# Performance work log

Measured on AMD Instinct MI355X. Metric: run time of the kernel, lower is better.

The kernel has to match this reference:

```python
import jax, jax.numpy as jnp
import numpy as np

B, N, C_IN, C_OUT, E_DIM = 16, 1024, 64, 64, 4


def setup_inputs() -> dict:
    key = jax.random.key(0)
    ks = jax.random.split(key, 7)
    x = jax.random.normal(ks[0], (B, N, C_IN), dtype=jnp.float32)
    adj = jax.random.uniform(ks[1], (B, N, N), dtype=jnp.float32)
    edge_attr = jax.random.randint(ks[2], (B, N, N, 1), 0, E_DIM, dtype=jnp.int32)
    scale = 1.0 / np.sqrt(C_IN)
    W_rel = jax.random.normal(ks[3], (C_IN, C_OUT), dtype=jnp.float32) * scale
    b_rel = jax.random.normal(ks[4], (C_OUT,), dtype=jnp.float32) * scale
    W_root = jax.random.normal(ks[5], (C_IN, C_OUT), dtype=jnp.float32) * scale
    w_edge = jax.random.normal(ks[6], (E_DIM,), dtype=jnp.float32)
    return {"x": x, "adj": adj, "edge_attr": edge_attr,
            "W_rel": W_rel, "b_rel": b_rel, "W_root": W_root, "w_edge": w_edge}


def reference(x, adj, edge_attr, W_rel, b_rel, W_root, w_edge):
    # one_hot(edge_attr) @ w_edge == gather of w_edge by edge type (same math,
    # avoids materializing the B x N x N x E_DIM one-hot tensor).
    e = w_edge[edge_attr[..., 0]]            # [B, N, N]
    adj_w = adj * e                           # weighted adjacency
    out = jnp.matmul(adj_w, x)                # [B, N, C_IN] aggregation (aggr='add')
    out = jnp.matmul(out, W_rel) + b_rel      # lin_rel
    out = out + jnp.matmul(x, W_root)         # lin_root (no bias)
    return out
```

## Files before the change

### kernel.cpp

```cpp
#include <hip/hip_runtime.h>

#define BB 16
#define NN 1024
#define CC 64

typedef __attribute__((ext_vector_type(8))) short short8;
typedef __attribute__((ext_vector_type(4))) float f32x4;
typedef __attribute__((ext_vector_type(4))) int   i32x4;

__device__ __forceinline__ unsigned short bf16_rne(float f) {
    unsigned u = __float_as_uint(f);
    u += 0x7fffu + ((u >> 16) & 1u);
    return (unsigned short)(u >> 16);
}

extern "C" __global__ __launch_bounds__(256)
void precompute(const float* __restrict__ x, const float* __restrict__ W_rel,
                const float* __restrict__ W_root, const float* __restrict__ b_rel,
                unsigned short* __restrict__ xw_sw, float* __restrict__ out)
{
    __shared__ float wrel_s[64 * 64];
    __shared__ float wroot_s[64 * 64];
    __shared__ float x_s[16 * 68];

    const int t = threadIdx.x;
    #pragma unroll
    for (int k = 0; k < 4; ++k) {
        int i4 = t + 256 * k;
        ((float4*)wrel_s)[i4]  = ((const float4*)W_rel)[i4];
        ((float4*)wroot_s)[i4] = ((const float4*)W_root)[i4];
    }
    const int row0 = blockIdx.x * 16;
    {
        int r = t >> 4, c4 = t & 15;
        *(float4*)(x_s + r * 68 + c4 * 4) = ((const float4*)(x + (size_t)(row0 + r) * CC))[c4];
    }
    __syncthreads();

    const int c4 = t & 15;
    const int r  = t >> 4;
    float aw0 = 0.f, aw1 = 0.f, aw2 = 0.f, aw3 = 0.f;
    float ar0 = 0.f, ar1 = 0.f, ar2 = 0.f, ar3 = 0.f;
    const float* xrow = x_s + r * 68;
    #pragma unroll 8
    for (int k = 0; k < 64; ++k) {
        float xv = xrow[k];
        float4 wv = ((const float4*)(wrel_s  + k * 64))[c4];
        float4 rv = ((const float4*)(wroot_s + k * 64))[c4];
        aw0 += xv * wv.x; aw1 += xv * wv.y; aw2 += xv * wv.z; aw3 += xv * wv.w;
        ar0 += xv * rv.x; ar1 += xv * rv.y; ar2 += xv * rv.z; ar3 += xv * rv.w;
    }

    const int row_g = row0 + r;
    {
        const float4 bv = ((const float4*)b_rel)[c4];
        ((float4*)out)[(size_t)row_g * 16 + c4] =
            make_float4(ar0 + bv.x, ar1 + bv.y, ar2 + bv.z, ar3 + bv.w);
    }
    {
        const int b = row_g >> 10;
        const int k = row_g & 1023;
        const int kb = k >> 5;
        const int qk = (k >> 3) & 3;
        const int j  = k & 7;
        const int c  = 4 * c4;
        const int n0 = c >> 4;
        const int n  = c & 15;
        size_t off = ((size_t)b << 16) + (size_t)((kb * 4 + n0) << 9)
                   + (size_t)((n + (qk << 4)) << 3) + j;
        xw_sw[off]      = bf16_rne(aw0);
        xw_sw[off + 8]  = bf16_rne(aw1);
        xw_sw[off + 16] = bf16_rne(aw2);
        xw_sw[off + 24] = bf16_rne(aw3);
    }
}

extern "C" __global__ __launch_bounds__(256, 4)
void gnn_mfma(const float* __restrict__ adj, const int* __restrict__ ea,
              const float* __restrict__ w_edge,
              const unsigned short* __restrict__ xw_sw,
              float* __restrict__ out)
{
    __shared__ __align__(16) char lds[32768];

    const int t     = threadIdx.x;
    const int mtile = blockIdx.x & 63;
    const int b     = blockIdx.x >> 6;
    const int row0  = mtile << 4;

    const float w0 = w_edge[0], w1 = w_edge[1], w2 = w_edge[2], w3 = w_edge[3];
    const float d1 = w1 - w0;
    const float d2 = w2 - 2.f * w1 + w0;
    const float d3 = w3 - 3.f * w2 + 3.f * w1 - w0;
    const float c3 = d3 * (1.f / 6.f);
    const float c2 = 0.5f * d2 - 0.5f * d3;
    const float c1 = d1 - 0.5f * d2 + (1.f / 3.f) * d3;
    const float c0 = w0;

#define WSEL(ev) __builtin_fmaf(__builtin_fmaf(__builtin_fmaf(c3, (float)(ev), c2), (float)(ev), c1), (float)(ev), c0)

    const size_t gbase = ((size_t)b << 20) + ((size_t)row0 << 10);
    const f32x4* A4 = (const f32x4*)(adj + gbase);
    const i32x4* E4 = (const i32x4*)(ea + gbase);

    const int kb_t   = t >> 3;
    const int q_t    = (t >> 1) & 3;
    const int X_t    = ((kb_t & 3) << 2) | q_t;
    const int wbase  = (kb_t << 10) + (q_t << 8) + ((t & 1) << 3);

    f32x4 aa[8]; i32x4 ee[8];
    #pragma unroll
    for (int d = 0; d < 8; ++d) {
        aa[d] = __builtin_nontemporal_load(&A4[d * 256 + t]);
        ee[d] = __builtin_nontemporal_load(&E4[d * 256 + t]);
    }

    #pragma unroll
    for (int i = 0; i < 16; ++i) {
        f32x4 av = aa[i & 7];
        i32x4 ev = ee[i & 7];
        if (i < 8) {
            aa[i & 7] = __builtin_nontemporal_load(&A4[(i + 8) * 256 + t]);
            ee[i & 7] = __builtin_nontemporal_load(&E4[(i + 8) * 256 + t]);
        }
        float p0 = av[0] * WSEL(ev[0]);
        float p1 = av[1] * WSEL(ev[1]);
        float p2 = av[2] * WSEL(ev[2]);
        float p3 = av[3] * WSEL(ev[3]);
        unsigned u0 = __builtin_amdgcn_perm(__float_as_uint(p1), __float_as_uint(p0), 0x07060302u);
        unsigned u1 = __builtin_amdgcn_perm(__float_as_uint(p3), __float_as_uint(p2), 0x07060302u);
        const int m = i;
        const int addr = wbase + ((m ^ X_t) << 4);
        *(uint2*)(lds + addr) = make_uint2(u0, u1);
    }
    __syncthreads();

    const int wn   = t >> 6;
    const int lane = t & 63;
    const int m    = lane & 15;
    const int q    = lane >> 4;

    const unsigned short* xwb = xw_sw + ((size_t)b << 16)
                              + ((size_t)wn << 9) + ((size_t)lane << 3);
    const char* abase = lds + (q << 8);

    f32x4 acc0 = {0.f, 0.f, 0.f, 0.f};

    #pragma unroll
    for (int kb = 0; kb < 32; ++kb) {
        const int X = ((kb & 3) << 2) | q;
        short8 af = *(const short8*)(abase + (kb << 10) + ((m ^ X) << 4));
        short8 bf = *(const short8*)(xwb + ((size_t)kb << 11));
        acc0 = __builtin_amdgcn_mfma_f32_16x16x32_bf16(af, bf, acc0, 0, 0, 0);
    }
#undef WSEL

    float* ob = out + ((((size_t)b << 10) + row0 + (q << 2)) << 6) + (wn << 4) + m;
    #pragma unroll
    for (int rg = 0; rg < 4; ++rg) {
        ob[rg * 64] += acc0[rg];
    }
}

extern "C" void kernel_launch(void* const* d_in, const int* in_sizes, int n_in,
                              void* d_out, int out_size, void* d_ws, size_t ws_size,
                              hipStream_t stream) {
    const float* x      = (const float*)d_in[0];
    const float* adj    = (const float*)d_in[1];
    const int*   ea     = (const int*)  d_in[2];
    const float* W_rel  = (const float*)d_in[3];
    const float* b_rel  = (const float*)d_in[4];
    const float* W_root = (const float*)d_in[5];
    const float* w_edge = (const float*)d_in[6];
    float* out = (float*)d_out;

    unsigned short* xw_sw = (unsigned short*)d_ws;

    precompute<<<BB * NN / 16, 256, 0, stream>>>(x, W_rel, W_root, b_rel, xw_sw, out);
    gnn_mfma<<<BB * (NN / 16), 256, 0, stream>>>(adj, ea, w_edge, xw_sw, out);
}
```

Baseline: 164.9 us.

## Split adjacency weighting into a separate bf16 pack pass before the MFMA kernel

Adds a streaming pack kernel that reads adj and edge_attr, applies the edge-type weights, and writes a bf16 weighted adjacency to workspace. A lighter MFMA kernel then reads the packed bf16 rows directly, with no LDS staging. The aim is better memory streaming and occupancy in each pass. The cost is an extra 32 MB write and read round trip plus one more kernel launch, on top of the mandatory 128 MB input read. The original fused path is kept as a fallback when the workspace is too small.

```diff
diff --git a/kernel.cpp b/kernel.cpp
--- a/kernel.cpp
+++ b/kernel.cpp
@@ -13,6 +13,17 @@
     u += 0x7fffu + ((u >> 16) & 1u);
     return (unsigned short)(u >> 16);
 }
+
+#define WSEL_COEFFS(w_edge) \
+    const float w0 = w_edge[0], w1 = w_edge[1], w2 = w_edge[2], w3 = w_edge[3]; \
+    const float d1 = w1 - w0; \
+    const float d2 = w2 - 2.f * w1 + w0; \
+    const float d3 = w3 - 3.f * w2 + 3.f * w1 - w0; \
+    const float c3 = d3 * (1.f / 6.f); \
+    const float c2 = 0.5f * d2 - 0.5f * d3; \
+    const float c1 = d1 - 0.5f * d2 + (1.f / 3.f) * d3; \
+    const float c0 = w0;
+#define WSEL(ev) __builtin_fmaf(__builtin_fmaf(__builtin_fmaf(c3, (float)(ev), c2), (float)(ev), c1), (float)(ev), c0)
 
 extern "C" __global__ __launch_bounds__(256)
 void precompute(const float* __restrict__ x, const float* __restrict__ W_rel,
@@ -75,6 +86,78 @@
     }
 }
 
+extern "C" __global__ __launch_bounds__(256)
+void pack(const float* __restrict__ adj, const int* __restrict__ ea,
+          const float* __restrict__ w_edge, uint2* __restrict__ adjw)
+{
+    const int g = blockIdx.x * 256 + threadIdx.x;
+    const int S = 2048 * 256;
+
+    WSEL_COEFFS(w_edge);
+
+    const f32x4* A4 = (const f32x4*)adj;
+    const i32x4* E4 = (const i32x4*)ea;
+
+    f32x4 a[4]; i32x4 e[4];
+    #pragma unroll
+    for (int j = 0; j < 4; ++j) {
+        a[j] = __builtin_nontemporal_load(&A4[(size_t)j * S + g]);
+        e[j] = __builtin_nontemporal_load(&E4[(size_t)j * S + g]);
+    }
+
+    #pragma unroll
+    for (int j = 0; j < 8; ++j) {
+        f32x4 av = a[j & 3];
+        i32x4 ev = e[j & 3];
+        if (j < 4) {
+            a[j & 3] = __builtin_nontemporal_load(&A4[(size_t)(j + 4) * S + g]);
+            e[j & 3] = __builtin_nontemporal_load(&E4[(size_t)(j + 4) * S + g]);
+        }
+        float p0 = av[0] * WSEL(ev[0]);
+        float p1 = av[1] * WSEL(ev[1]);
+        float p2 = av[2] * WSEL(ev[2]);
+        float p3 = av[3] * WSEL(ev[3]);
+        unsigned u0 = __builtin_amdgcn_perm(__float_as_uint(p1), __float_as_uint(p0), 0x07060302u);
+        unsigned u1 = __builtin_amdgcn_perm(__float_as_uint(p3), __float_as_uint(p2), 0x07060302u);
+        adjw[(size_t)j * S + g] = make_uint2(u0, u1);
+    }
+}
+
+extern "C" __global__ __launch_bounds__(256)
+void gnn_lite(const unsigned short* __restrict__ adjw,
+              const unsigned short* __restrict__ xw_sw,
+              float* __restrict__ out)
+{
+    const int t     = threadIdx.x;
+    const int wn    = t >> 6;
+    const int lane  = t & 63;
+    const int m     = lane & 15;
+    const int q     = lane >> 4;
+    const int mtile = blockIdx.x & 63;
+    const int b     = blockIdx.x >> 6;
+    const int row0  = mtile << 4;
+
+    const unsigned short* ap = adjw + ((size_t)b << 20)
+                             + ((size_t)(row0 + m) << 10) + (q << 3);
+    const unsigned short* xwb = xw_sw + ((size_t)b << 16)
+                              + ((size_t)wn << 9) + ((size_t)lane << 3);
+
+    f32x4 acc = {0.f, 0.f, 0.f, 0.f};
+
+    #pragma unroll
+    for (int kb = 0; kb < 32; ++kb) {
+        short8 af = *(const short8*)(ap + (kb << 5));
+        short8 bf = *(const short8*)(xwb + ((size_t)kb << 11));
+        acc = __builtin_amdgcn_mfma_f32_16x16x32_bf16(af, bf, acc, 0, 0, 0);
+    }
+
+    float* ob = out + ((((size_t)b << 10) + row0 + (q << 2)) << 6) + (wn << 4) + m;
+    #pragma unroll
+    for (int rg = 0; rg < 4; ++rg) {
+        ob[rg * 64] += acc[rg];
+    }
+}
+
 extern "C" __global__ __launch_bounds__(256, 4)
 void gnn_mfma(const float* __restrict__ adj, const int* __restrict__ ea,
               const float* __restrict__ w_edge,
@@ -88,16 +171,7 @@
     const int b     = blockIdx.x >> 6;
     const int row0  = mtile << 4;
 
-    const float w0 = w_edge[0], w1 = w_edge[1], w2 = w_edge[2], w3 = w_edge[3];
-    const float d1 = w1 - w0;
-    const float d2 = w2 - 2.f * w1 + w0;
-    const float d3 = w3 - 3.f * w2 + 3.f * w1 - w0;
-    const float c3 = d3 * (1.f / 6.f);
-    const float c2 = 0.5f * d2 - 0.5f * d3;
-    const float c1 = d1 - 0.5f * d2 + (1.f / 3.f) * d3;
-    const float c0 = w0;
-
-#define WSEL(ev) __builtin_fmaf(__builtin_fmaf(__builtin_fmaf(c3, (float)(ev), c2), (float)(ev), c1), (float)(ev), c0)
+    WSEL_COEFFS(w_edge);
 
     const size_t gbase = ((size_t)b << 20) + ((size_t)row0 << 10);
     const f32x4* A4 = (const f32x4*)(adj + gbase);
@@ -153,7 +227,6 @@
         short8 bf = *(const short8*)(xwb + ((size_t)kb << 11));
         acc0 = __builtin_amdgcn_mfma_f32_16x16x32_bf16(af, bf, acc0, 0, 0, 0);
     }
-#undef WSEL
 
     float* ob = out + ((((size_t)b << 10) + row0 + (q << 2)) << 6) + (wn << 4) + m;
     #pragma unroll
@@ -177,5 +250,13 @@
     unsigned short* xw_sw = (unsigned short*)d_ws;
 
     precompute<<<BB * NN / 16, 256, 0, stream>>>(x, W_rel, W_root, b_rel, xw_sw, out);
-    gnn_mfma<<<BB * (NN / 16), 256, 0, stream>>>(adj, ea, w_edge, xw_sw, out);
-}
+
+    const size_t need = ((size_t)1 << 22) + ((size_t)32 << 20);
+    if (ws_size >= need) {
+        uint2* adjw = (uint2*)((char*)d_ws + ((size_t)1 << 22));
+        pack<<<2048, 256, 0, stream>>>(adj, ea, w_edge, adjw);
+        gnn_lite<<<BB * (NN / 16), 256, 0, stream>>>((const unsigned short*)adjw, xw_sw, out);
+    } else {
+        gnn_mfma<<<BB * (NN / 16), 256, 0, stream>>>(adj, ea, w_edge, xw_sw, out);
+    }
+}
```

New measurement: 184.5 us. +11.9%, slower.
